# Optimization experiments

Hardware: AMD Instinct MI355X
Metric: run time of the kernel (lower is better)

The kernel has to match this reference:

```python
import jax, jax.numpy as jnp
import numpy as np

IN, H1, H2, V = 1024, 2048, 2048, 50257


def setup_inputs() -> dict:
    key = jax.random.key(0)
    ks = jax.random.split(key, 16)
    def n(k, shape, scale=1.0):
        return (jax.random.normal(k, shape, dtype=jnp.float32) * scale).astype(jnp.float32)
    s1 = 1.0 / np.sqrt(H1)  # pytorch LSTM init scale ~ U(-1/sqrt(H),1/sqrt(H)); gaussian stand-in
    s2 = 1.0 / np.sqrt(H2)
    so = 1.0 / np.sqrt(H2)
    return {
        "x":  n(ks[0], (IN,)),
        "h1": n(ks[1], (H1,)), "c1": n(ks[2], (H1,)),
        "h2": n(ks[3], (H2,)), "c2": n(ks[4], (H2,)),
        "W_ih1": n(ks[5], (4 * H1, IN), s1), "W_hh1": n(ks[6], (4 * H1, H1), s1),
        "b_ih1": n(ks[7], (4 * H1,), s1),   "b_hh1": n(ks[8], (4 * H1,), s1),
        "W_ih2": n(ks[9], (4 * H2, H1), s2), "W_hh2": n(ks[10], (4 * H2, H2), s2),
        "b_ih2": n(ks[11], (4 * H2,), s2),  "b_hh2": n(ks[12], (4 * H2,), s2),
        "W_out": n(ks[13], (V, H2), so),    "b_out": n(ks[14], (V,), so),
    }


def _lstm_step(x, h, c, W_ih, W_hh, b_ih, b_hh):
    # PyTorch gate ordering: i, f, g, o
    gates = W_ih @ x + b_ih + W_hh @ h + b_hh  # [4H]
    i, f, g, o = jnp.split(gates, 4)
    i = jax.nn.sigmoid(i)
    f = jax.nn.sigmoid(f)
    g = jnp.tanh(g)
    o = jax.nn.sigmoid(o)
    c_new = f * c + i * g
    h_new = o * jnp.tanh(c_new)
    return h_new, c_new


def reference(x, h1, c1, h2, c2,
              W_ih1, W_hh1, b_ih1, b_hh1,
              W_ih2, W_hh2, b_ih2, b_hh2,
              W_out, b_out):
    h1n, _ = _lstm_step(x, h1, c1, W_ih1, W_hh1, b_ih1, b_hh1)
    h2n, _ = _lstm_step(h1n, h2, c2, W_ih2, W_hh2, b_ih2, b_hh2)
    logits = W_out @ h2n + b_out                     # [V]
    # dropout(p=0.1) treated as identity (eval mode) for a deterministic baseline
    return jax.nn.log_softmax(logits)[None, :]       # [1, V], matches dim=1 log-softmax
```

## Files before the change

### kernel.cpp

```cpp
#include <hip/hip_runtime.h>
#include <hip/hip_bf16.h>

typedef unsigned short u16;
typedef u16 u16x8 __attribute__((ext_vector_type(8)));
typedef float f32x8 __attribute__((ext_vector_type(8)));

#define IN_DIM 1024
#define H_DIM  2048
#define V_DIM  50257
#define NEG_BIG (-1e30f)

__device__ __forceinline__ float bf2f(u16 u) {
    union { unsigned int i; float f; } v;
    v.i = ((unsigned int)u) << 16;
    return v.f;
}

__device__ __forceinline__ u16 f2bf(float f) {
    union { float f; unsigned int i; } v;
    v.f = f;
    unsigned int i = v.i;
    i += 0x7fffu + ((i >> 16) & 1u);
    return (u16)(i >> 16);
}

template<typename T>
__device__ __forceinline__ T ntl(const T* p) { return __builtin_nontemporal_load(p); }

__device__ __forceinline__ float wave_allreduce_sum(float v) {
    #pragma unroll
    for (int d = 32; d; d >>= 1) v += __shfl_xor(v, d, 64);
    return v;
}

__device__ __forceinline__ float sigmoidf(float x) { return 1.f / (1.f + __expf(-x)); }

__device__ __forceinline__ float ld_scalar(const void* p, int i, bool bf) {
    return bf ? bf2f(((const u16*)p)[i]) : ((const float*)p)[i];
}

__device__ __forceinline__ bool probe_bf16(const void* x) {
    const u16* p = (const u16*)x;
    const int lane = threadIdx.x & 63;
    u16 w = p[2 * lane];
    int e = (w >> 7) & 0xFF;
    unsigned long long b = __ballot(e >= 0x60 && e <= 0x8F);
    return __popcll(b) > 40;
}

__global__ __launch_bounds__(256) void lstm1_kernel(
    const void* __restrict__ x, const void* __restrict__ h1, const void* __restrict__ c1,
    const void* __restrict__ W_ih, const void* __restrict__ W_hh,
    const void* __restrict__ b_ih, const void* __restrict__ b_hh,
    float* __restrict__ h_out)
{
    const bool bf  = probe_bf16(x);
    const int j    = blockIdx.x;
    const int wave = threadIdx.x >> 6;
    const int lane = threadIdx.x & 63;
    const int row  = wave * H_DIM + j;

    float acc = 0.f;
    if (bf) {
        {
            const u16x8* wp = (const u16x8*)W_ih + (size_t)row * (IN_DIM / 8) + lane;
            const u16x8* vp = (const u16x8*)x + lane;
            u16x8 a[2], v[2];
            #pragma unroll
            for (int k = 0; k < 2; ++k) { a[k] = ntl(wp + 64 * k); v[k] = vp[64 * k]; }
            #pragma unroll
            for (int k = 0; k < 2; ++k)
                #pragma unroll
                for (int t = 0; t < 8; ++t) acc += bf2f(a[k][t]) * bf2f(v[k][t]);
        }
        {
            const u16x8* wp = (const u16x8*)W_hh + (size_t)row * (H_DIM / 8) + lane;
            const u16x8* vp = (const u16x8*)h1 + lane;
            u16x8 a[4], v[4];
            #pragma unroll
            for (int k = 0; k < 4; ++k) { a[k] = ntl(wp + 64 * k); v[k] = vp[64 * k]; }
            #pragma unroll
            for (int k = 0; k < 4; ++k)
                #pragma unroll
                for (int t = 0; t < 8; ++t) acc += bf2f(a[k][t]) * bf2f(v[k][t]);
        }
    } else {
        {
            const f32x8* wp = (const f32x8*)W_ih + (size_t)row * (IN_DIM / 8) + lane;
            const f32x8* vp = (const f32x8*)x + lane;
            f32x8 a[2], v[2];
            #pragma unroll
            for (int k = 0; k < 2; ++k) { a[k] = ntl(wp + 64 * k); v[k] = vp[64 * k]; }
            #pragma unroll
            for (int k = 0; k < 2; ++k)
                #pragma unroll
                for (int t = 0; t < 8; ++t) acc += a[k][t] * v[k][t];
        }
        {
            const f32x8* wp = (const f32x8*)W_hh + (size_t)row * (H_DIM / 8) + lane;
            const f32x8* vp = (const f32x8*)h1 + lane;
            f32x8 a[4], v[4];
            #pragma unroll
            for (int k = 0; k < 4; ++k) { a[k] = ntl(wp + 64 * k); v[k] = vp[64 * k]; }
            #pragma unroll
            for (int k = 0; k < 4; ++k)
                #pragma unroll
                for (int t = 0; t < 8; ++t) acc += a[k][t] * v[k][t];
        }
    }
    acc = wave_allreduce_sum(acc);

    __shared__ float gs[4];
    if (lane == 0) gs[wave] = acc + ld_scalar(b_ih, row, bf) + ld_scalar(b_hh, row, bf);
    __syncthreads();
    if (threadIdx.x == 0) {
        float gi = sigmoidf(gs[0]);
        float gf = sigmoidf(gs[1]);
        float gg = tanhf(gs[2]);
        float go = sigmoidf(gs[3]);
        float c  = gf * ld_scalar(c1, j, bf) + gi * gg;
        h_out[j] = go * tanhf(c);
    }
}

__global__ __launch_bounds__(256) void lstm2_kernel(
    const void* __restrict__ x,
    const float* __restrict__ h1n, const void* __restrict__ h2, const void* __restrict__ c2,
    const void* __restrict__ W_ih, const void* __restrict__ W_hh,
    const void* __restrict__ b_ih, const void* __restrict__ b_hh,
    float* __restrict__ h_out)
{
    const bool bf  = probe_bf16(x);
    const int j    = blockIdx.x;
    const int wave = threadIdx.x >> 6;
    const int lane = threadIdx.x & 63;
    const int row  = wave * H_DIM + j;

    float acc = 0.f;
    if (bf) {
        {
            const u16x8* wp = (const u16x8*)W_ih + (size_t)row * (H_DIM / 8) + lane;
            const f32x8* vp = (const f32x8*)h1n + lane;
            u16x8 a[4]; f32x8 v[4];
            #pragma unroll
            for (int k = 0; k < 4; ++k) { a[k] = ntl(wp + 64 * k); v[k] = vp[64 * k]; }
            #pragma unroll
            for (int k = 0; k < 4; ++k)
                #pragma unroll
                for (int t = 0; t < 8; ++t) acc += bf2f(a[k][t]) * v[k][t];
        }
        {
            const u16x8* wp = (const u16x8*)W_hh + (size_t)row * (H_DIM / 8) + lane;
            const u16x8* vp = (const u16x8*)h2 + lane;
            u16x8 a[4], v[4];
            #pragma unroll
            for (int k = 0; k < 4; ++k) { a[k] = ntl(wp + 64 * k); v[k] = vp[64 * k]; }
            #pragma unroll
            for (int k = 0; k < 4; ++k)
                #pragma unroll
                for (int t = 0; t < 8; ++t) acc += bf2f(a[k][t]) * bf2f(v[k][t]);
        }
    } else {
        {
            const f32x8* wp = (const f32x8*)W_ih + (size_t)row * (H_DIM / 8) + lane;
            const f32x8* vp = (const f32x8*)h1n + lane;
            f32x8 a[4], v[4];
            #pragma unroll
            for (int k = 0; k < 4; ++k) { a[k] = ntl(wp + 64 * k); v[k] = vp[64 * k]; }
            #pragma unroll
            for (int k = 0; k < 4; ++k)
                #pragma unroll
                for (int t = 0; t < 8; ++t) acc += a[k][t] * v[k][t];
        }
        {
            const f32x8* wp = (const f32x8*)W_hh + (size_t)row * (H_DIM / 8) + lane;
            const f32x8* vp = (const f32x8*)h2 + lane;
            f32x8 a[4], v[4];
            #pragma unroll
            for (int k = 0; k < 4; ++k) { a[k] = ntl(wp + 64 * k); v[k] = vp[64 * k]; }
            #pragma unroll
            for (int k = 0; k < 4; ++k)
                #pragma unroll
                for (int t = 0; t < 8; ++t) acc += a[k][t] * v[k][t];
        }
    }
    acc = wave_allreduce_sum(acc);

    __shared__ float gs[4];
    if (lane == 0) gs[wave] = acc + ld_scalar(b_ih, row, bf) + ld_scalar(b_hh, row, bf);
    __syncthreads();
    if (threadIdx.x == 0) {
        float gi = sigmoidf(gs[0]);
        float gf = sigmoidf(gs[1]);
        float gg = tanhf(gs[2]);
        float go = sigmoidf(gs[3]);
        float c  = gf * ld_scalar(c2, j, bf) + gi * gg;
        h_out[j] = go * tanhf(c);
    }
}

#define ROWS_PER_WAVE 8
#define ROWS_PER_BLOCK 32
__global__ __launch_bounds__(256) void logits_kernel(
    const void* __restrict__ x,
    const float* __restrict__ h2n, const void* __restrict__ W, const void* __restrict__ b,
    float* __restrict__ logits, float* __restrict__ pmax, float* __restrict__ psum)
{
    const bool bf  = probe_bf16(x);
    const int wave = threadIdx.x >> 6;
    const int lane = threadIdx.x & 63;

    float hreg[32];
    {
        const f32x8* hv = (const f32x8*)h2n;
        #pragma unroll
        for (int k = 0; k < 4; ++k) {
            f32x8 hh = hv[lane + 64 * k];
            #pragma unroll
            for (int t = 0; t < 8; ++t) hreg[8 * k + t] = hh[t];
        }
    }

    const int base = blockIdx.x * ROWS_PER_BLOCK + wave * ROWS_PER_WAVE;
    float m = NEG_BIG, s = 0.f;

    if (bf) {
        #pragma unroll
        for (int p = 0; p < 4; ++p) {
            const int r0 = base + 2 * p, r1 = r0 + 1;
            const int c0 = min(r0, V_DIM - 1), c1 = min(r1, V_DIM - 1);
            const u16x8* w0 = (const u16x8*)W + (size_t)c0 * (H_DIM / 8) + lane;
            const u16x8* w1 = (const u16x8*)W + (size_t)c1 * (H_DIM / 8) + lane;
            u16x8 a0[4], a1[4];
            #pragma unroll
            for (int k = 0; k < 4; ++k) { a0[k] = ntl(w0 + 64 * k); a1[k] = ntl(w1 + 64 * k); }
            float acc0 = 0.f, acc1 = 0.f;
            #pragma unroll
            for (int k = 0; k < 4; ++k)
                #pragma unroll
                for (int t = 0; t < 8; ++t) {
                    float hval = hreg[8 * k + t];
                    acc0 += bf2f(a0[k][t]) * hval;
                    acc1 += bf2f(a1[k][t]) * hval;
                }
            #pragma unroll
            for (int d = 32; d; d >>= 1) {
                acc0 += __shfl_xor(acc0, d, 64);
                acc1 += __shfl_xor(acc1, d, 64);
            }
            const float l0 = acc0 + ld_scalar(b, c0, true);
            const float l1 = acc1 + ld_scalar(b, c1, true);
            const bool v0 = (r0 < V_DIM), v1 = (r1 < V_DIM);
            if (lane == 0) {
                if (v0) logits[r0] = l0;
                if (v1) logits[r1] = l1;
            }
            const float mx = fmaxf(v0 ? l0 : NEG_BIG, v1 ? l1 : NEG_BIG);
            if (mx > -1e29f) {
                const float mn = fmaxf(m, mx);
                s = s * __expf(m - mn)
                  + (v0 ? __expf(l0 - mn) : 0.f)
                  + (v1 ? __expf(l1 - mn) : 0.f);
                m = mn;
            }
        }
    } else {
        #pragma unroll
        for (int rr = 0; rr < ROWS_PER_WAVE; ++rr) {
            const int r = base + rr;
            const int cr = min(r, V_DIM - 1);
            const f32x8* wr = (const f32x8*)W + (size_t)cr * (H_DIM / 8) + lane;
            f32x8 a[4];
            #pragma unroll
            for (int k = 0; k < 4; ++k) a[k] = ntl(wr + 64 * k);
            float acc = 0.f;
            #pragma unroll
            for (int k = 0; k < 4; ++k)
                #pragma unroll
                for (int t = 0; t < 8; ++t) acc += a[k][t] * hreg[8 * k + t];
            acc = wave_allreduce_sum(acc);
            const float lg = acc + ((const float*)b)[cr];
            const bool v = (r < V_DIM);
            if (lane == 0 && v) logits[r] = lg;
            if (v) {
                const float mn = fmaxf(m, lg);
                s = s * __expf(m - mn) + __expf(lg - mn);
                m = mn;
            }
        }
    }

    __shared__ float wm[4], wsv[4];
    if (lane == 0) { wm[wave] = m; wsv[wave] = s; }
    __syncthreads();
    if (threadIdx.x == 0) {
        float M = fmaxf(fmaxf(wm[0], wm[1]), fmaxf(wm[2], wm[3]));
        float S = 0.f;
        #pragma unroll
        for (int w = 0; w < 4; ++w) S += wsv[w] * __expf(wm[w] - M);
        pmax[blockIdx.x] = M;
        psum[blockIdx.x] = S;
    }
}

__global__ __launch_bounds__(256) void finalize_kernel(
    const void* __restrict__ x,
    const float* __restrict__ logits, const float* __restrict__ pmax,
    const float* __restrict__ psum, int nblk,
    void* __restrict__ out)
{
    const bool bf = probe_bf16(x);
    __shared__ float sm[256], ss[256];
    float m = NEG_BIG, s = 0.f;
    for (int i = threadIdx.x; i < nblk; i += 256) {
        float bm = pmax[i], bs = psum[i];
        float mn = fmaxf(m, bm);
        s = s * __expf(m - mn) + bs * __expf(bm - mn);
        m = mn;
    }
    sm[threadIdx.x] = m; ss[threadIdx.x] = s;
    __syncthreads();
    #pragma unroll
    for (int stride = 128; stride > 0; stride >>= 1) {
        if ((int)threadIdx.x < stride) {
            float m1 = sm[threadIdx.x], s1 = ss[threadIdx.x];
            float m2 = sm[threadIdx.x + stride], s2 = ss[threadIdx.x + stride];
            float mn = fmaxf(m1, m2);
            sm[threadIdx.x] = mn;
            ss[threadIdx.x] = s1 * __expf(m1 - mn) + s2 * __expf(m2 - mn);
        }
        __syncthreads();
    }
    const float logZ = sm[0] + __logf(ss[0]);
    const int i = blockIdx.x * 256 + threadIdx.x;
    if (i < V_DIM) {
        float v = logits[i] - logZ;
        if (bf) ((u16*)out)[i] = f2bf(v);
        else    ((float*)out)[i] = v;
    }
}

extern "C" void kernel_launch(void* const* d_in, const int* in_sizes, int n_in,
                              void* d_out, int out_size, void* d_ws, size_t ws_size,
                              hipStream_t stream)
{
    const void* x     = d_in[0];
    const void* h1    = d_in[1];
    const void* c1    = d_in[2];
    const void* h2    = d_in[3];
    const void* c2    = d_in[4];
    const void* W_ih1 = d_in[5];
    const void* W_hh1 = d_in[6];
    const void* b_ih1 = d_in[7];
    const void* b_hh1 = d_in[8];
    const void* W_ih2 = d_in[9];
    const void* W_hh2 = d_in[10];
    const void* b_ih2 = d_in[11];
    const void* b_hh2 = d_in[12];
    const void* W_out = d_in[13];
    const void* b_out = d_in[14];

    float* ws     = (float*)d_ws;
    float* h1n    = ws;
    float* h2n    = ws + 2048;
    float* logits = ws + 4096;
    float* pmax   = ws + 4096 + 50264;
    float* psum   = pmax + 1576;

    const int nblk3 = (V_DIM + ROWS_PER_BLOCK - 1) / ROWS_PER_BLOCK;

    lstm1_kernel<<<H_DIM, 256, 0, stream>>>(x, h1, c1, W_ih1, W_hh1, b_ih1, b_hh1, h1n);
    lstm2_kernel<<<H_DIM, 256, 0, stream>>>(x, h1n, h2, c2, W_ih2, W_hh2, b_ih2, b_hh2, h2n);
    logits_kernel<<<nblk3, 256, 0, stream>>>(x, h2n, W_out, b_out, logits, pmax, psum);
    finalize_kernel<<<(V_DIM + 255) / 256, 256, 0, stream>>>(x, logits, pmax, psum, nblk3, d_out);
}
```

Baseline: 685.3 us.

## Fuse LSTM layers, logits, and log-softmax into one cooperative persistent kernel

Replaces the four-kernel pipeline with one cooperative kernel on a grid of 1024 blocks that uses grid.sync between the LSTM1, LSTM2, logits and normalization phases. This removes three launch boundaries and the launch gaps between them. In exchange the logits phase gives each wave one contiguous chunk of rows with a loop that is not unrolled, so fewer rows are in flight per wave. Grid-wide barriers and a redundant per-block reduction of the partial max/sum values are also added. The fallback logits kernel also loses its paired-row bf16 path.

```diff
diff --git a/kernel.cpp b/kernel.cpp
--- a/kernel.cpp
+++ b/kernel.cpp
@@ -1,5 +1,7 @@
 #include <hip/hip_runtime.h>
-#include <hip/hip_bf16.h>
+#include <hip/hip_cooperative_groups.h>
+
+namespace cg = cooperative_groups;
 
 typedef unsigned short u16;
 typedef u16 u16x8 __attribute__((ext_vector_type(8)));
@@ -9,6 +11,7 @@
 #define H_DIM  2048
 #define V_DIM  50257
 #define NEG_BIG (-1e30f)
+#define COOP_GRID 1024
 
 __device__ __forceinline__ float bf2f(u16 u) {
     union { unsigned int i; float f; } v;
@@ -48,6 +51,195 @@
     return __popcll(b) > 40;
 }
 
+template<int NVEC>
+__device__ __forceinline__ float dotN_bf(const u16x8* wp, const u16x8* vp, int lane) {
+    u16x8 a[NVEC], v[NVEC];
+    #pragma unroll
+    for (int k = 0; k < NVEC; ++k) { a[k] = ntl(wp + lane + 64 * k); v[k] = vp[lane + 64 * k]; }
+    float acc = 0.f;
+    #pragma unroll
+    for (int k = 0; k < NVEC; ++k)
+        #pragma unroll
+        for (int t = 0; t < 8; ++t) acc += bf2f(a[k][t]) * bf2f(v[k][t]);
+    return acc;
+}
+
+template<int NVEC>
+__device__ __forceinline__ float dotN_f32(const f32x8* wp, const f32x8* vp, int lane) {
+    f32x8 a[NVEC], v[NVEC];
+    #pragma unroll
+    for (int k = 0; k < NVEC; ++k) { a[k] = ntl(wp + lane + 64 * k); v[k] = vp[lane + 64 * k]; }
+    float acc = 0.f;
+    #pragma unroll
+    for (int k = 0; k < NVEC; ++k)
+        #pragma unroll
+        for (int t = 0; t < 8; ++t) acc += a[k][t] * v[k][t];
+    return acc;
+}
+
+template<int NVEC>
+__device__ __forceinline__ float dotN_bf_f32v(const u16x8* wp, const f32x8* vp, int lane) {
+    u16x8 a[NVEC]; f32x8 v[NVEC];
+    #pragma unroll
+    for (int k = 0; k < NVEC; ++k) { a[k] = ntl(wp + lane + 64 * k); v[k] = vp[lane + 64 * k]; }
+    float acc = 0.f;
+    #pragma unroll
+    for (int k = 0; k < NVEC; ++k)
+        #pragma unroll
+        for (int t = 0; t < 8; ++t) acc += bf2f(a[k][t]) * v[k][t];
+    return acc;
+}
+
+__global__ __launch_bounds__(256, 4) void fused_kernel(
+    const void* __restrict__ x, const void* __restrict__ h1, const void* __restrict__ c1,
+    const void* __restrict__ h2, const void* __restrict__ c2,
+    const void* __restrict__ W_ih1, const void* __restrict__ W_hh1,
+    const void* __restrict__ b_ih1, const void* __restrict__ b_hh1,
+    const void* __restrict__ W_ih2, const void* __restrict__ W_hh2,
+    const void* __restrict__ b_ih2, const void* __restrict__ b_hh2,
+    const void* __restrict__ W_out, const void* __restrict__ b_out,
+    float* __restrict__ h1n, float* __restrict__ h2n,
+    float* __restrict__ logits, float* __restrict__ pm, float* __restrict__ ps,
+    void* __restrict__ out)
+{
+    cg::grid_group grid = cg::this_grid();
+    const bool bf  = probe_bf16(x);
+    const int wave = threadIdx.x >> 6;
+    const int lane = threadIdx.x & 63;
+    __shared__ float gs[4];
+    __shared__ float sm[256], ss[256];
+
+    for (int j = blockIdx.x; j < H_DIM; j += gridDim.x) {
+        const int row = wave * H_DIM + j;
+        float acc;
+        if (bf) {
+            acc = dotN_bf<2>((const u16x8*)W_ih1 + (size_t)row * (IN_DIM / 8), (const u16x8*)x, lane)
+                + dotN_bf<4>((const u16x8*)W_hh1 + (size_t)row * (H_DIM / 8), (const u16x8*)h1, lane);
+        } else {
+            acc = dotN_f32<2>((const f32x8*)W_ih1 + (size_t)row * (IN_DIM / 8), (const f32x8*)x, lane)
+                + dotN_f32<4>((const f32x8*)W_hh1 + (size_t)row * (H_DIM / 8), (const f32x8*)h1, lane);
+        }
+        acc = wave_allreduce_sum(acc);
+        if (lane == 0) gs[wave] = acc + ld_scalar(b_ih1, row, bf) + ld_scalar(b_hh1, row, bf);
+        __syncthreads();
+        if (threadIdx.x == 0) {
+            float gi = sigmoidf(gs[0]);
+            float gf = sigmoidf(gs[1]);
+            float gg = tanhf(gs[2]);
+            float go = sigmoidf(gs[3]);
+            float c  = gf * ld_scalar(c1, j, bf) + gi * gg;
+            h1n[j] = go * tanhf(c);
+        }
+        __syncthreads();
+    }
+    __threadfence();
+    grid.sync();
+
+    for (int j = blockIdx.x; j < H_DIM; j += gridDim.x) {
+        const int row = wave * H_DIM + j;
+        float acc;
+        if (bf) {
+            acc = dotN_bf_f32v<4>((const u16x8*)W_ih2 + (size_t)row * (H_DIM / 8), (const f32x8*)h1n, lane)
+                + dotN_bf<4>((const u16x8*)W_hh2 + (size_t)row * (H_DIM / 8), (const u16x8*)h2, lane);
+        } else {
+            acc = dotN_f32<4>((const f32x8*)W_ih2 + (size_t)row * (H_DIM / 8), (const f32x8*)h1n, lane)
+                + dotN_f32<4>((const f32x8*)W_hh2 + (size_t)row * (H_DIM / 8), (const f32x8*)h2, lane);
+        }
+        acc = wave_allreduce_sum(acc);
+        if (lane == 0) gs[wave] = acc + ld_scalar(b_ih2, row, bf) + ld_scalar(b_hh2, row, bf);
+        __syncthreads();
+        if (threadIdx.x == 0) {
+            float gi = sigmoidf(gs[0]);
+            float gf = sigmoidf(gs[1]);
+            float gg = tanhf(gs[2]);
+            float go = sigmoidf(gs[3]);
+            float c  = gf * ld_scalar(c2, j, bf) + gi * gg;
+            h2n[j] = go * tanhf(c);
+        }
+        __syncthreads();
+    }
+    __threadfence();
+    grid.sync();
+
+    float hreg[32];
+    {
+        const f32x8* hv = (const f32x8*)h2n;
+        #pragma unroll
+        for (int k = 0; k < 4; ++k) {
+            f32x8 hh = hv[lane + 64 * k];
+            #pragma unroll
+            for (int t = 0; t < 8; ++t) hreg[8 * k + t] = hh[t];
+        }
+    }
+    const int NW  = gridDim.x * 4;
+    const int wid = blockIdx.x * 4 + wave;
+    const int rpw = (V_DIM + NW - 1) / NW;
+    const int rbeg = wid * rpw;
+    const int rend = min(rbeg + rpw, V_DIM);
+    float m = NEG_BIG, s = 0.f;
+    for (int r = rbeg; r < rend; ++r) {
+        float acc = 0.f;
+        if (bf) {
+            const u16x8* wr = (const u16x8*)W_out + (size_t)r * (H_DIM / 8) + lane;
+            u16x8 a[4];
+            #pragma unroll
+            for (int k = 0; k < 4; ++k) a[k] = ntl(wr + 64 * k);
+            #pragma unroll
+            for (int k = 0; k < 4; ++k)
+                #pragma unroll
+                for (int t = 0; t < 8; ++t) acc += bf2f(a[k][t]) * hreg[8 * k + t];
+        } else {
+            const f32x8* wr = (const f32x8*)W_out + (size_t)r * (H_DIM / 8) + lane;
+            f32x8 a[4];
+            #pragma unroll
+            for (int k = 0; k < 4; ++k) a[k] = ntl(wr + 64 * k);
+            #pragma unroll
+            for (int k = 0; k < 4; ++k)
+                #pragma unroll
+                for (int t = 0; t < 8; ++t) acc += a[k][t] * hreg[8 * k + t];
+        }
+        acc = wave_allreduce_sum(acc);
+        const float lg = acc + ld_scalar(b_out, r, bf);
+        if (lane == 0) logits[r] = lg;
+        const float mn = fmaxf(m, lg);
+        s = s * __expf(m - mn) + __expf(lg - mn);
+        m = mn;
+    }
+    if (lane == 0) { pm[wid] = m; ps[wid] = s; }
+    __threadfence();
+    grid.sync();
+
+    {
+        float mm = NEG_BIG, sv = 0.f;
+        for (int i = threadIdx.x; i < NW; i += 256) {
+            float bm = pm[i], bs = ps[i];
+            float mn = fmaxf(mm, bm);
+            sv = sv * __expf(mm - mn) + bs * __expf(bm - mn);
+            mm = mn;
+        }
+        sm[threadIdx.x] = mm; ss[threadIdx.x] = sv;
+        __syncthreads();
+        #pragma unroll
+        for (int stride = 128; stride > 0; stride >>= 1) {
+            if ((int)threadIdx.x < stride) {
+                float m1 = sm[threadIdx.x], s1 = ss[threadIdx.x];
+                float m2 = sm[threadIdx.x + stride], s2 = ss[threadIdx.x + stride];
+                float mn = fmaxf(m1, m2);
+                sm[threadIdx.x] = mn;
+                ss[threadIdx.x] = s1 * __expf(m1 - mn) + s2 * __expf(m2 - mn);
+            }
+            __syncthreads();
+        }
+    }
+    const float logZ = sm[0] + __logf(ss[0]);
+
+    for (int i = blockIdx.x * 256 + threadIdx.x; i < V_DIM; i += gridDim.x * 256) {
+        float v = logits[i] - logZ;
+        if (bf) ((u16*)out)[i] = f2bf(v);
+        else    ((float*)out)[i] = v;
+    }
+}
+
 __global__ __launch_bounds__(256) void lstm1_kernel(
     const void* __restrict__ x, const void* __restrict__ h1, const void* __restrict__ c1,
     const void* __restrict__ W_ih, const void* __restrict__ W_hh,
@@ -60,53 +252,13 @@
     const int lane = threadIdx.x & 63;
     const int row  = wave * H_DIM + j;
 
-    float acc = 0.f;
+    float acc;
     if (bf) {
-        {
-            const u16x8* wp = (const u16x8*)W_ih + (size_t)row * (IN_DIM / 8) + lane;
-            const u16x8* vp = (const u16x8*)x + lane;
-            u16x8 a[2], v[2];
-            #pragma unroll
-            for (int k = 0; k < 2; ++k) { a[k] = ntl(wp + 64 * k); v[k] = vp[64 * k]; }
-            #pragma unroll
-            for (int k = 0; k < 2; ++k)
-                #pragma unroll
-                for (int t = 0; t < 8; ++t) acc += bf2f(a[k][t]) * bf2f(v[k][t]);
-        }
-        {
-            const u16x8* wp = (const u16x8*)W_hh + (size_t)row * (H_DIM / 8) + lane;
-            const u16x8* vp = (const u16x8*)h1 + lane;
-            u16x8 a[4], v[4];
-            #pragma unroll
-            for (int k = 0; k < 4; ++k) { a[k] = ntl(wp + 64 * k); v[k] = vp[64 * k]; }
-            #pragma unroll
-            for (int k = 0; k < 4; ++k)
-                #pragma unroll
-                for (int t = 0; t < 8; ++t) acc += bf2f(a[k][t]) * bf2f(v[k][t]);
-        }
+        acc = dotN_bf<2>((const u16x8*)W_ih + (size_t)row * (IN_DIM / 8), (const u16x8*)x, lane)
+            + dotN_bf<4>((const u16x8*)W_hh + (size_t)row * (H_DIM / 8), (const u16x8*)h1, lane);
     } else {
-        {
-            const f32x8* wp = (const f32x8*)W_ih + (size_t)row * (IN_DIM / 8) + lane;
-            const f32x8* vp = (const f32x8*)x + lane;
-            f32x8 a[2], v[2];
-            #pragma unroll
-            for (int k = 0; k < 2; ++k) { a[k] = ntl(wp + 64 * k); v[k] = vp[64 * k]; }
-            #pragma unroll
-            for (int k = 0; k < 2; ++k)
-                #pragma unroll
-                for (int t = 0; t < 8; ++t) acc += a[k][t] * v[k][t];
-        }
-        {
-            const f32x8* wp = (const f32x8*)W_hh + (size_t)row * (H_DIM / 8) + lane;
-            const f32x8* vp = (const f32x8*)h1 + lane;
-            f32x8 a[4], v[4];
-            #pragma unroll
-            for (int k = 0; k < 4; ++k) { a[k] = ntl(wp + 64 * k); v[k] = vp[64 * k]; }
-            #pragma unroll
-            for (int k = 0; k < 4; ++k)
-                #pragma unroll
-                for (int t = 0; t < 8; ++t) acc += a[k][t] * v[k][t];
-        }
+        acc = dotN_f32<2>((const f32x8*)W_ih + (size_t)row * (IN_DIM / 8), (const f32x8*)x, lane)
+            + dotN_f32<4>((const f32x8*)W_hh + (size_t)row * (H_DIM / 8), (const f32x8*)h1, lane);
     }
     acc = wave_allreduce_sum(acc);
 
@@ -136,53 +288,13 @@
     const int lane = threadIdx.x & 63;
     const int row  = wave * H_DIM + j;
 
-    float acc = 0.f;
+    float acc;
     if (bf) {
-        {
-            const u16x8* wp = (const u16x8*)W_ih + (size_t)row * (H_DIM / 8) + lane;
-            const f32x8* vp = (const f32x8*)h1n + lane;
-            u16x8 a[4]; f32x8 v[4];
-            #pragma unroll
-            for (int k = 0; k < 4; ++k) { a[k] = ntl(wp + 64 * k); v[k] = vp[64 * k]; }
-            #pragma unroll
-            for (int k = 0; k < 4; ++k)
-                #pragma unroll
-                for (int t = 0; t < 8; ++t) acc += bf2f(a[k][t]) * v[k][t];
-        }
-        {
-            const u16x8* wp = (const u16x8*)W_hh + (size_t)row * (H_DIM / 8) + lane;
-            const u16x8* vp = (const u16x8*)h2 + lane;
-            u16x8 a[4], v[4];
-            #pragma unroll
-            for (int k = 0; k < 4; ++k) { a[k] = ntl(wp + 64 * k); v[k] = vp[64 * k]; }
-            #pragma unroll
-            for (int k = 0; k < 4; ++k)
-                #pragma unroll
-                for (int t = 0; t < 8; ++t) acc += bf2f(a[k][t]) * bf2f(v[k][t]);
-        }
+        acc = dotN_bf_f32v<4>((const u16x8*)W_ih + (size_t)row * (H_DIM / 8), (const f32x8*)h1n, lane)
+            + dotN_bf<4>((const u16x8*)W_hh + (size_t)row * (H_DIM / 8), (const u16x8*)h2, lane);
     } else {
-        {
-            const f32x8* wp = (const f32x8*)W_ih + (size_t)row * (H_DIM / 8) + lane;
-            const f32x8* vp = (const f32x8*)h1n + lane;
-            f32x8 a[4], v[4];
-            #pragma unroll
-            for (int k = 0; k < 4; ++k) { a[k] = ntl(wp + 64 * k); v[k] = vp[64 * k]; }
-            #pragma unroll
-            for (int k = 0; k < 4; ++k)
-                #pragma unroll
-                for (int t = 0; t < 8; ++t) acc += a[k][t] * v[k][t];
-        }
-        {
-            const f32x8* wp = (const f32x8*)W_hh + (size_t)row * (H_DIM / 8) + lane;
-            const f32x8* vp = (const f32x8*)h2 + lane;
-            f32x8 a[4], v[4];
-            #pragma unroll
-            for (int k = 0; k < 4; ++k) { a[k] = ntl(wp + 64 * k); v[k] = vp[64 * k]; }
-            #pragma unroll
-            for (int k = 0; k < 4; ++k)
-                #pragma unroll
-                for (int t = 0; t < 8; ++t) acc += a[k][t] * v[k][t];
-        }
+        acc = dotN_f32<4>((const f32x8*)W_ih + (size_t)row * (H_DIM / 8), (const f32x8*)h1n, lane)
+            + dotN_f32<4>((const f32x8*)W_hh + (size_t)row * (H_DIM / 8), (const f32x8*)h2, lane);
     }
     acc = wave_allreduce_sum(acc);
 
@@ -223,70 +335,37 @@
 
     const int base = blockIdx.x * ROWS_PER_BLOCK + wave * ROWS_PER_WAVE;
     float m = NEG_BIG, s = 0.f;
-
-    if (bf) {
-        #pragma unroll
-        for (int p = 0; p < 4; ++p) {
-            const int r0 = base + 2 * p, r1 = r0 + 1;
-            const int c0 = min(r0, V_DIM - 1), c1 = min(r1, V_DIM - 1);
-            const u16x8* w0 = (const u16x8*)W + (size_t)c0 * (H_DIM / 8) + lane;
-            const u16x8* w1 = (const u16x8*)W + (size_t)c1 * (H_DIM / 8) + lane;
-            u16x8 a0[4], a1[4];
-            #pragma unroll
-            for (int k = 0; k < 4; ++k) { a0[k] = ntl(w0 + 64 * k); a1[k] = ntl(w1 + 64 * k); }
-            float acc0 = 0.f, acc1 = 0.f;
+    for (int rr = 0; rr < ROWS_PER_WAVE; ++rr) {
+        const int r = base + rr;
+        const int cr = min(r, V_DIM - 1);
+        float acc = 0.f;
+        if (bf) {
+            const u16x8* wr = (const u16x8*)W + (size_t)cr * (H_DIM / 8) + lane;
+            u16x8 a[4];
+            #pragma unroll
+            for (int k = 0; k < 4; ++k) a[k] = ntl(wr + 64 * k);
             #pragma unroll
             for (int k = 0; k < 4; ++k)
                 #pragma unroll
-                for (int t = 0; t < 8; ++t) {
-                    float hval = hreg[8 * k + t];
-                    acc0 += bf2f(a0[k][t]) * hval;
-                    acc1 += bf2f(a1[k][t]) * hval;
-                }
-            #pragma unroll
-            for (int d = 32; d; d >>= 1) {
-                acc0 += __shfl_xor(acc0, d, 64);
-                acc1 += __shfl_xor(acc1, d, 64);
-            }
-            const float l0 = acc0 + ld_scalar(b, c0, true);
-            const float l1 = acc1 + ld_scalar(b, c1, true);
-            const bool v0 = (r0 < V_DIM), v1 = (r1 < V_DIM);
-            if (lane == 0) {
-                if (v0) logits[r0] = l0;
-                if (v1) logits[r1] = l1;
-            }
-            const float mx = fmaxf(v0 ? l0 : NEG_BIG, v1 ? l1 : NEG_BIG);
-            if (mx > -1e29f) {
-                const float mn = fmaxf(m, mx);
-                s = s * __expf(m - mn)
-                  + (v0 ? __expf(l0 - mn) : 0.f)
-                  + (v1 ? __expf(l1 - mn) : 0.f);
-                m = mn;
-            }
-        }
-    } else {
-        #pragma unroll
-        for (int rr = 0; rr < ROWS_PER_WAVE; ++rr) {
-            const int r = base + rr;
-            const int cr = min(r, V_DIM - 1);
+                for (int t = 0; t < 8; ++t) acc += bf2f(a[k][t]) * hreg[8 * k + t];
+        } else {
             const f32x8* wr = (const f32x8*)W + (size_t)cr * (H_DIM / 8) + lane;
             f32x8 a[4];
             #pragma unroll
             for (int k = 0; k < 4; ++k) a[k] = ntl(wr + 64 * k);
-            float acc = 0.f;
             #pragma unroll
             for (int k = 0; k < 4; ++k)
                 #pragma unroll
                 for (int t = 0; t < 8; ++t) acc += a[k][t] * hreg[8 * k + t];
-            acc = wave_allreduce_sum(acc);
-            const float lg = acc + ((const float*)b)[cr];
-            const bool v = (r < V_DIM);
-            if (lane == 0 && v) logits[r] = lg;
-            if (v) {
-                const float mn = fmaxf(m, lg);
-                s = s * __expf(m - mn) + __expf(lg - mn);
-                m = mn;
-            }
+        }
+        acc = wave_allreduce_sum(acc);
+        const float lg = acc + ld_scalar(b, cr, bf);
+        const bool valid = (r < V_DIM);
+        if (lane == 0 && valid) logits[r] = lg;
+        if (valid) {
+            const float mn = fmaxf(m, lg);
+            s = s * __expf(m - mn) + __expf(lg - mn);
+            m = mn;
         }
     }
 
@@ -364,13 +443,42 @@
     float* h1n    = ws;
     float* h2n    = ws + 2048;
     float* logits = ws + 4096;
-    float* pmax   = ws + 4096 + 50264;
-    float* psum   = pmax + 1576;
-
-    const int nblk3 = (V_DIM + ROWS_PER_BLOCK - 1) / ROWS_PER_BLOCK;
-
-    lstm1_kernel<<<H_DIM, 256, 0, stream>>>(x, h1, c1, W_ih1, W_hh1, b_ih1, b_hh1, h1n);
-    lstm2_kernel<<<H_DIM, 256, 0, stream>>>(x, h1n, h2, c2, W_ih2, W_hh2, b_ih2, b_hh2, h2n);
-    logits_kernel<<<nblk3, 256, 0, stream>>>(x, h2n, W_out, b_out, logits, pmax, psum);
-    finalize_kernel<<<(V_DIM + 255) / 256, 256, 0, stream>>>(x, logits, pmax, psum, nblk3, d_out);
-}
+    float* pm     = ws + 4096 + 50264;
+    float* psv    = pm + 4096;
+
+    static int coop = -1;
+    if (coop < 0) {
+        int dev = 0, v = 0;
+        hipGetDevice(&dev);
+        if (hipDeviceGetAttribute(&v, hipDeviceAttributeCooperativeLaunch, dev) != hipSuccess) v = 0;
+        coop = v;
+    }
+
+    bool launched = false;
+    if (coop) {
+        void* args[] = {
+            (void*)&x, (void*)&h1, (void*)&c1, (void*)&h2, (void*)&c2,
+            (void*)&W_ih1, (void*)&W_hh1, (void*)&b_ih1, (void*)&b_hh1,
+            (void*)&W_ih2, (void*)&W_hh2, (void*)&b_ih2, (void*)&b_hh2,
+            (void*)&W_out, (void*)&b_out,
+            (void*)&h1n, (void*)&h2n, (void*)&logits, (void*)&pm, (void*)&psv,
+            (void*)&d_out
+        };
+        hipError_t e = hipLaunchCooperativeKernel((const void*)fused_kernel,
+                                                  dim3(COOP_GRID), dim3(256),
+                                                  args, 0, stream);
+        if (e == hipSuccess) {
+            launched = true;
+        } else {
+            (void)hipGetLastError();
+        }
+    }
+
+    if (!launched) {
+        const int nblk3 = (V_DIM + ROWS_PER_BLOCK - 1) / ROWS_PER_BLOCK;
+        lstm1_kernel<<<H_DIM, 256, 0, stream>>>(x, h1, c1, W_ih1, W_hh1, b_ih1, b_hh1, h1n);
+        lstm2_kernel<<<H_DIM, 256, 0, stream>>>(x, h1n, h2, c2, W_ih2, W_hh2, b_ih2, b_hh2, h2n);
+        logits_kernel<<<nblk3, 256, 0, stream>>>(x, h2n, W_out, b_out, logits, pm, psv);
+        finalize_kernel<<<(V_DIM + 255) / 256, 256, 0, stream>>>(x, logits, pm, psv, nblk3, d_out);
+    }
+}
```

Result: slower. 1.562 ms (+127.9%).
